# Performance work log

Measured on AMD Instinct MI355X. Metric: run time of the kernel, lower is better.

Reference implementation:

```python
import jax, jax.numpy as jnp
import numpy as np

B, S, T, E, H, VIN, VOUT = 64, 64, 32, 512, 1024, 32000, 32000


def setup_inputs() -> dict:
    key = jax.random.key(0)
    ks = jax.random.split(key, 12)
    rn = lambda k, shape, s=0.02: jax.random.normal(k, shape, jnp.float32) * s
    return {
        "src": jax.random.randint(ks[0], (B, S), 0, VIN),
        "tgt": jax.random.randint(ks[1], (B, T), 0, VOUT),
        "enc_emb": rn(ks[2], (VIN, E)),
        "dec_emb": rn(ks[3], (VOUT, E)),
        "enc_Wih": rn(ks[4], (4 * H, E)),
        "enc_Whh": rn(ks[5], (4 * H, H)),
        "enc_bih": jnp.zeros((4 * H,), jnp.float32),
        "enc_bhh": jnp.zeros((4 * H,), jnp.float32),
        "dec_Wih": rn(ks[6], (4 * H, E + H)),
        "dec_Whh": rn(ks[7], (4 * H, H)),
        "dec_bih": jnp.zeros((4 * H,), jnp.float32),
        "dec_bhh": jnp.zeros((4 * H,), jnp.float32),
        "attn_W": rn(ks[8], (H, 2 * H)),
        "attn_b": jnp.zeros((H,), jnp.float32),
        "v": jax.random.uniform(ks[9], (H,), jnp.float32),
        "fc_W": rn(ks[10], (VOUT, 2 * H)),
        "fc_b": jnp.zeros((VOUT,), jnp.float32),
    }


def _lstm_cell(x, h, c, Wih, Whh, bih, bhh):
    # torch gate order: i, f, g, o
    gates = x @ Wih.T + bih + h @ Whh.T + bhh
    i, f, g, o = jnp.split(gates, 4, axis=-1)
    c_new = jax.nn.sigmoid(f) * c + jax.nn.sigmoid(i) * jnp.tanh(g)
    h_new = jax.nn.sigmoid(o) * jnp.tanh(c_new)
    return h_new, c_new


def _forward(src, tgt, enc_emb, dec_emb, enc_Wih, enc_Whh, enc_bih, enc_bhh,
             dec_Wih, dec_Whh, dec_bih, dec_bhh, attn_W, attn_b, v, fc_W, fc_b):
    b, s = src.shape
    t_len = tgt.shape[1]
    hdim = enc_Whh.shape[1]

    # ---- encoder (single-layer LSTM, batch_first) ----
    x = enc_emb[src]  # [B,S,E] (dropout=0 in eval)

    def enc_step(carry, x_t):
        h, c = carry
        h, c = _lstm_cell(x_t, h, c, enc_Wih, enc_Whh, enc_bih, enc_bhh)
        return (h, c), h

    h0 = jnp.zeros((b, hdim), x.dtype)
    (h_f, c_f), enc_out_tm = jax.lax.scan(enc_step, (h0, h0), jnp.swapaxes(x, 0, 1))
    enc_out = jnp.swapaxes(enc_out_tm, 0, 1)  # [B,S,H]

    # hidden.detach() in torch
    h_f = jax.lax.stop_gradient(h_f)
    c_f = jax.lax.stop_gradient(c_f)

    # split attn_W for the concat(hidden, enc_out) linear
    Wh, We = attn_W[:, :hdim], attn_W[:, hdim:]
    enc_proj = jnp.einsum('bsh,kh->bsk', enc_out, We)  # hoisted, [B,S,H]

    def dec_step(carry, tok):
        h, c = carry
        emb = dec_emb[tok]  # [B,E]
        # Bahdanau attention: tanh(Linear(cat(h, enc_out))) . v
        energy = jnp.tanh(h @ Wh.T[None] if False else jnp.tanh((h @ Wh.T)[:, None, :] + enc_proj + attn_b))
        energy = jnp.tanh((h @ Wh.T)[:, None, :] + enc_proj + attn_b)  # [B,S,H]
        scores = jnp.einsum('bsh,h->bs', energy, v)
        a = jax.nn.softmax(scores, axis=1)
        context = jnp.einsum('bs,bsh->bh', a, enc_out)  # [B,H]
        rnn_in = jnp.concatenate([emb, context], axis=-1)
        h_new, c_new = _lstm_cell(rnn_in, h, c, dec_Wih, dec_Whh, dec_bih, dec_bhh)
        logits = jnp.concatenate([h_new, context], axis=-1) @ fc_W.T + fc_b
        return (h_new, c_new), logits

    # teacher_forcing_ratio = 1.0 -> input at step t is tgt[:, t-1]
    toks_tm = jnp.swapaxes(tgt[:, : t_len - 1], 0, 1)  # [T-1, B]
    _, logits_tm = jax.lax.scan(dec_step, (h_f, c_f), toks_tm)  # [T-1,B,V]
    logits = jnp.swapaxes(logits_tm, 0, 1)  # [B,T-1,V]
    zeros0 = jnp.zeros((b, 1, fc_W.shape[0]), logits.dtype)
    return jnp.concatenate([zeros0, logits], axis=1)  # [B,T,V]


def reference(src, tgt, enc_emb, dec_emb, enc_Wih, enc_Whh, enc_bih, enc_bhh,
              dec_Wih, dec_Whh, dec_bih, dec_bhh, attn_W, attn_b, v, fc_W, fc_b):
    return _forward(src, tgt, enc_emb, dec_emb, enc_Wih, enc_Whh, enc_bih, enc_bhh,
                    dec_Wih, dec_Whh, dec_bih, dec_bhh, attn_W, attn_b, v, fc_W, fc_b)
```

## Files before the change

### kernel.cpp

```cpp
#include <hip/hip_runtime.h>
#include <hip/hip_bf16.h>

typedef __bf16 bf16x8 __attribute__((ext_vector_type(8)));
typedef float  f32x4  __attribute__((ext_vector_type(4)));
typedef _Float16 h16x8 __attribute__((ext_vector_type(8)));

__device__ __forceinline__ unsigned short f2b(float f) {
    union { float f; unsigned u; } w; w.f = f;
    unsigned u = w.u + 0x7FFF + ((w.u >> 16) & 1);
    return (unsigned short)(u >> 16);
}
__device__ __forceinline__ float tanhfast(float x) {
    float e = __expf(2.0f * x);
    return 1.0f - 2.0f / (e + 1.0f);
}

__device__ __forceinline__ void stU(unsigned* p, unsigned v) {
    __hip_atomic_store(p, v, __ATOMIC_RELAXED, __HIP_MEMORY_SCOPE_AGENT);
}
__device__ __forceinline__ void stF(float* p, float v) {
    __hip_atomic_store(p, v, __ATOMIC_RELAXED, __HIP_MEMORY_SCOPE_AGENT);
}
__device__ __forceinline__ int ldI(const int* p) {
    return __hip_atomic_load((int*)p, __ATOMIC_RELAXED, __HIP_MEMORY_SCOPE_AGENT);
}
__device__ __forceinline__ void stI(int* p, int v) {
    __hip_atomic_store(p, v, __ATOMIC_RELAXED, __HIP_MEMORY_SCOPE_AGENT);
}

#define GLD16(g, l) __builtin_amdgcn_global_load_lds( \
    (const __attribute__((address_space(1))) void*)(g), \
    (__attribute__((address_space(3))) void*)(l), 16, 0, 0)

#define SLOT_STRIDE 16

__device__ __forceinline__ void gbar(int* slots, int* gen, int target) {
    asm volatile("s_waitcnt vmcnt(0)" ::: "memory");
    __syncthreads();
    if (blockIdx.x == 0) {
        if (threadIdx.x == 0) stI(slots, target);
        while (ldI(slots + threadIdx.x * SLOT_STRIDE) < target)
            __builtin_amdgcn_s_sleep(1);
        __syncthreads();
        if (threadIdx.x == 0) stI(gen, target);
    } else {
        if (threadIdx.x == 0) {
            stI(slots + blockIdx.x * SLOT_STRIDE, target);
            while (ldI(gen) < target)
                __builtin_amdgcn_s_sleep(1);
        }
        __syncthreads();
    }
}

__device__ __forceinline__ void mac8(const unsigned short* A, const unsigned short* B,
                                     f32x4& acc) {
    bf16x8 a[8], b[8];
#pragma unroll
    for (int kk = 0; kk < 8; ++kk) {
        a[kk] = *(const bf16x8*)(A + kk * 32);
        b[kk] = *(const bf16x8*)(B + kk * 32);
    }
#pragma unroll
    for (int kk = 0; kk < 8; ++kk)
        acc = __builtin_amdgcn_mfma_f32_16x16x32_bf16(a[kk], b[kk], acc, 0, 0, 0);
}


__global__ void k_gather(const float* __restrict__ emb, const int* __restrict__ tok,
                         unsigned short* __restrict__ out, int L, int ldtok) {
    long total = (long)L * 64 * 128;
    for (long i = (long)blockIdx.x * blockDim.x + threadIdx.x; i < total;
         i += (long)gridDim.x * blockDim.x) {
        int  e4 = (int)(i & 127);
        long r  = i >> 7;
        int  t  = (int)(r >> 6), b = (int)(r & 63);
        int  tk = tok[b * ldtok + t];
        float4 v = *(const float4*)(emb + (long)tk * 512 + e4 * 4);
        ushort4 o; o.x = f2b(v.x); o.y = f2b(v.y); o.z = f2b(v.z); o.w = f2b(v.w);
        *(ushort4*)(out + r * 512 + e4 * 4) = o;
    }
}

__global__ void k_conv(const float* __restrict__ in, unsigned short* __restrict__ out,
                       long N_, int K_, int ldin, int col0, int ldout, int outcol0, int reorder) {
    long total = N_ * (K_ >> 2);
    int kq = K_ >> 2;
    for (long i = (long)blockIdx.x * blockDim.x + threadIdx.x; i < total;
         i += (long)gridDim.x * blockDim.x) {
        long n = i / kq;
        int  k4 = (int)(i - n * kq) * 4;
        long row = reorder ? (long)((n & 3) * 1024 + (n >> 2)) : n;
        float4 v = *(const float4*)(in + row * ldin + col0 + k4);
        ushort4 o; o.x = f2b(v.x); o.y = f2b(v.y); o.z = f2b(v.z); o.w = f2b(v.w);
        *(ushort4*)(out + n * ldout + outcol0 + k4) = o;
    }
}

__global__ void k_bias(const float* __restrict__ b1, const float* __restrict__ b2,
                       float* __restrict__ out) {
    int n = blockIdx.x * blockDim.x + threadIdx.x;
    if (n < 4096) {
        int row = (n & 3) * 1024 + (n >> 2);
        out[n] = b1[row] + b2[row];
    }
}

__global__ void k_zero0(float* __restrict__ out) {
    long total = 64L * 8000;
    for (long i = (long)blockIdx.x * blockDim.x + threadIdx.x; i < total;
         i += (long)gridDim.x * blockDim.x) {
        int b = (int)(i / 8000), q = (int)(i % 8000);
        float4 z = {0.f, 0.f, 0.f, 0.f};
        *(float4*)(out + (long)b * 1024000 + q * 4) = z;
    }
}

template<int BM, int BN, int WGM, int WGN, int FM, int FN>
__device__ __forceinline__ void gemm_core(
    const unsigned short* __restrict__ A, int lda,
    const unsigned short* __restrict__ B, int ldb,
    long m0, long n0, int K,
    unsigned short* As, unsigned short* Bs,
    f32x4 (&acc)[FM][FN])
{
    const int tid  = threadIdx.x;
    const int lane = tid & 63;
    const int wave = tid >> 6;
    const int wm = wave / WGN;
    const int wn = wave % WGN;
    const int srow = lane >> 2;
    const int scol = (lane & 3) * 8;
    const int frow = lane & 15;
    const int fcol = (lane >> 4) * 8;

    for (int k0 = 0; k0 < K; k0 += 32) {
        __syncthreads();
        for (int c = wave; c < BM / 16; c += 4) {
            const unsigned short* g = A + (m0 + c * 16 + srow) * (long)lda + k0 + scol;
            GLD16(g, As + c * 512);
        }
        for (int c = wave; c < BN / 16; c += 4) {
            const unsigned short* g = B + (n0 + c * 16 + srow) * (long)ldb + k0 + scol;
            GLD16(g, Bs + c * 512);
        }
        __syncthreads();
        bf16x8 af[FM], bfr[FN];
#pragma unroll
        for (int m = 0; m < FM; ++m)
            af[m] = *(const bf16x8*)(As + ((wm * FM + m) * 16 + frow) * 32 + fcol);
#pragma unroll
        for (int n = 0; n < FN; ++n)
            bfr[n] = *(const bf16x8*)(Bs + ((wn * FN + n) * 16 + frow) * 32 + fcol);
#pragma unroll
        for (int m = 0; m < FM; ++m)
#pragma unroll
            for (int n = 0; n < FN; ++n)
                acc[m][n] = __builtin_amdgcn_mfma_f32_16x16x32_bf16(af[m], bfr[n], acc[m][n], 0, 0, 0);
    }
}

template<int BM, int BN, int WGM, int WGN, int FM, int FN, int MODE>
__global__ __launch_bounds__(256) void k_gemm(
    const unsigned short* __restrict__ A, int lda,
    const unsigned short* __restrict__ B, int ldb,
    float* __restrict__ C, long ldc, const float* __restrict__ bias,
    int M, int N, int K, int Mreal)
{
    __shared__ __align__(16) unsigned short As[BM * 32];
    __shared__ __align__(16) unsigned short Bs[BN * 32];
    long m0, n0;
    if (MODE == 1) {
        int bid = blockIdx.x;
        int n = (bid & 7) * 32 + (bid >> 7);
        int m = (bid >> 3) & 15;
        if (n >= 250) return;
        m0 = (long)m * BM; n0 = (long)n * BN;
    } else {
        m0 = (long)blockIdx.y * BM; n0 = (long)blockIdx.x * BN;
    }
    f32x4 acc[FM][FN] = {};
    gemm_core<BM, BN, WGM, WGN, FM, FN>(A, lda, B, ldb, m0, n0, K, As, Bs, acc);

    const int lane = threadIdx.x & 63;
    const int wave = threadIdx.x >> 6;
    const int wm = wave / WGN, wn = wave % WGN;
#pragma unroll
    for (int n = 0; n < FN; ++n) {
        long col = n0 + wn * FN * 16 + n * 16 + (lane & 15);
        float bv = bias ? bias[col] : 0.0f;
#pragma unroll
        for (int m = 0; m < FM; ++m) {
            int rl = wm * FM * 16 + m * 16 + (lane >> 4) * 4;
#pragma unroll
            for (int q = 0; q < 4; ++q) {
                long r = m0 + rl + q;
                float val = acc[m][n][q] + bv;
                if (MODE == 0) {
                    C[r * ldc + col] = val;
                } else if (MODE == 2) {
                    ((_Float16*)C)[r * ldc + col] = (_Float16)val;
                } else {
                    if (r < Mreal) {
                        long orow = (r & 63) * 32 + (r >> 6) + 1;
                        C[orow * ldc + col] = val;
                    }
                }
            }
        }
    }
}

__global__ __launch_bounds__(256) void k_enc(
    const unsigned short* __restrict__ W,
    const float* __restrict__ pre,
    unsigned short* __restrict__ hsl,
    unsigned short* __restrict__ enc_out,
    unsigned short* __restrict__ eoT,
    unsigned short* __restrict__ hS0,
    float* __restrict__ cspill,
    int* slots, int* gen)
{
    __shared__ float gs[64 * 16];
    const int blk = blockIdx.x, tid = threadIdx.x;
    const int lane = tid & 63, wave = tid >> 6;
    const int n0 = blk * 16;
    const int arow = wave * 16 + (lane & 15);
    const int kch = (lane >> 4) * 8;
    const unsigned short* Bw = W + (long)(n0 + (lane & 15)) * 1024 + kch;
    const int pb = tid >> 1, pjl = (tid & 1) * 2;
    const int jg = blk * 4 + pjl;
    float c0 = 0.f, c1 = 0.f;
    float4 pr0 = {}, pr1 = {};
    if (tid < 128) {
        pr0 = *(const float4*)(pre + (long)pb * 4096 + n0 + pjl * 4);
        pr1 = *(const float4*)(pre + (long)pb * 4096 + n0 + pjl * 4 + 4);
    }
    int bt = 0;
    for (int t = 0; t < 64; ++t) {
        const unsigned short* Ar = hsl + (long)t * 65536 + (long)arow * 1024 + kch;
        f32x4 acc = {};
        mac8(Ar, Bw, acc);
        mac8(Ar + 256, Bw + 256, acc);
        mac8(Ar + 512, Bw + 512, acc);
        mac8(Ar + 768, Bw + 768, acc);
#pragma unroll
        for (int q = 0; q < 4; ++q)
            gs[(wave * 16 + (lane >> 4) * 4 + q) * 16 + (lane & 15)] = acc[q];
        __syncthreads();
        if (tid < 128) {
            float4 gA = *(const float4*)(gs + pb * 16 + pjl * 4);
            float4 gB = *(const float4*)(gs + pb * 16 + pjl * 4 + 4);
            float h0v, h1v;
            {
                float gi = gA.x + pr0.x, gf = gA.y + pr0.y, gg = gA.z + pr0.z, go = gA.w + pr0.w;
                float i_ = 1.f / (1.f + __expf(-gi)), f_ = 1.f / (1.f + __expf(-gf));
                float g_ = tanhfast(gg), o_ = 1.f / (1.f + __expf(-go));
                c0 = f_ * c0 + i_ * g_; h0v = o_ * tanhfast(c0);
            }
            {
                float gi = gB.x + pr1.x, gf = gB.y + pr1.y, gg = gB.z + pr1.z, go = gB.w + pr1.w;
                float i_ = 1.f / (1.f + __expf(-gi)), f_ = 1.f / (1.f + __expf(-gf));
                float g_ = tanhfast(gg), o_ = 1.f / (1.f + __expf(-go));
                c1 = f_ * c1 + i_ * g_; h1v = o_ * tanhfast(c1);
            }
            unsigned short hb0 = f2b(h0v), hb1 = f2b(h1v);
            unsigned pk = (unsigned)hb0 | ((unsigned)hb1 << 16);
            stU((unsigned*)(hsl + (long)(t + 1) * 65536 + (long)pb * 1024 + jg), pk);
            *(unsigned*)(enc_out + ((long)pb * 64 + t) * 1024 + jg) = pk;
            eoT[((long)pb * 1024 + jg) * 64 + t]     = hb0;
            eoT[((long)pb * 1024 + jg + 1) * 64 + t] = hb1;
            if (t < 63) {
                pr0 = *(const float4*)(pre + (long)(t + 1) * 262144 + (long)pb * 4096 + n0 + pjl * 4);
                pr1 = *(const float4*)(pre + (long)(t + 1) * 262144 + (long)pb * 4096 + n0 + pjl * 4 + 4);
            } else {
                *(unsigned*)(hS0 + (long)pb * 1024 + jg) = pk;
                cspill[(long)pb * 1024 + jg]     = c0;
                cspill[(long)pb * 1024 + jg + 1] = c1;
            }
        }
        gbar(slots, gen, ++bt);
    }
}

__global__ __launch_bounds__(256) void k_dec(
    const unsigned short* __restrict__ Wh,
    const unsigned short* __restrict__ Wc,
    const float* __restrict__ pre,
    const _Float16* __restrict__ proj16,
    const unsigned short* __restrict__ eoT,
    const float* __restrict__ v,
    const float* __restrict__ cspill,
    unsigned short* __restrict__ hS,
    unsigned short* __restrict__ ctxS,
    float* __restrict__ qS,
    unsigned short* __restrict__ fcin,
    int* slots, int* gen)
{
    __shared__ float gs[64 * 16];
    __shared__ float qv[1024], vv[1024];
    __shared__ float sc[64], al[64];
    const int blk = blockIdx.x, tid = threadIdx.x;
    const int lane = tid & 63, wave = tid >> 6;
    const int n0 = blk * 16;
    const int arow = wave * 16 + (lane & 15);
    const int kch = (lane >> 4) * 8;
    const int pb = tid >> 1, pjl = (tid & 1) * 2;
    const int jg = blk * 4 + pjl;
    {
        float4 v4 = *(const float4*)(v + tid * 4);
        *(float4*)(vv + tid * 4) = v4;
    }
    float c0 = 0.f, c1 = 0.f;
    if (tid < 128) {
        c0 = cspill[(long)pb * 1024 + jg];
        c1 = cspill[(long)pb * 1024 + jg + 1];
    }
    __syncthreads();
    int bt = 0;
    for (int t = 0; t < 31; ++t) {
        const unsigned short* hSt   = hS   + (long)t * 65536;
        const unsigned short* ctxSt = ctxS + (long)t * 65536;
        float4 pr0 = {}, pr1 = {};
        if (tid < 128) {
            pr0 = *(const float4*)(pre + (long)t * 262144 + (long)pb * 4096 + n0 + pjl * 4);
            pr1 = *(const float4*)(pre + (long)t * 262144 + (long)pb * 4096 + n0 + pjl * 4 + 4);
        }
        {
            int nq = blk >> 2, mt = blk & 3;
            gs[tid] = 0.f;
            __syncthreads();
            const unsigned short* Ar = hSt + (long)(mt * 16 + (lane & 15)) * 1024 + wave * 256 + kch;
            const unsigned short* Bq = Wh + (long)(nq * 16 + (lane & 15)) * 1024 + wave * 256 + kch;
            f32x4 qa = {};
            mac8(Ar, Bq, qa);
#pragma unroll
            for (int q = 0; q < 4; ++q)
                atomicAdd(&gs[((lane >> 4) * 4 + q) * 16 + (lane & 15)], qa[q]);
            __syncthreads();
            stF(qS + (long)t * 65536 + (long)(mt * 16 + (tid >> 4)) * 1024 + nq * 16 + (tid & 15),
                gs[tid]);
        }
        gbar(slots, gen, ++bt);
        if (blk < 64) {
            const int b = blk;
            *(float4*)(qv + tid * 4) = *(const float4*)(qS + (long)t * 65536 + (long)b * 1024 + tid * 4);
            __syncthreads();
            int s = tid >> 2, part = tid & 3;
            const h16x8* pp = (const h16x8*)(proj16 + ((long)b * 64 + s) * 1024 + part * 256);
            float a_ = 0.f;
#pragma unroll 4
            for (int d = 0; d < 32; ++d) {
                h16x8 pv = pp[d];
                int h = part * 256 + d * 8;
#pragma unroll
                for (int j = 0; j < 8; ++j)
                    a_ += vv[h + j] * tanhfast(qv[h + j] + (float)pv[j]);
            }
            a_ += __shfl_xor(a_, 1);
            a_ += __shfl_xor(a_, 2);
            if (part == 0) sc[s] = a_;
            __syncthreads();
            if (tid < 64) {
                float x = sc[tid], mx = x;
                for (int o = 32; o; o >>= 1) mx = fmaxf(mx, __shfl_xor(mx, o));
                float e = __expf(x - mx), su = e;
                for (int o = 32; o; o >>= 1) su += __shfl_xor(su, o);
                al[tid] = e / su;
            }
            __syncthreads();
            int h0 = tid * 4;
            float cacc[4];
#pragma unroll
            for (int r = 0; r < 4; ++r) {
                const bf16x8* ep = (const bf16x8*)(eoT + ((long)b * 1024 + h0 + r) * 64);
                float s_ = 0.f;
#pragma unroll
                for (int c8 = 0; c8 < 8; ++c8) {
                    bf16x8 v8 = ep[c8];
#pragma unroll
                    for (int jj = 0; jj < 8; ++jj)
                        s_ += al[c8 * 8 + jj] * (float)v8[jj];
                }
                cacc[r] = s_;
            }
            unsigned pk0 = (unsigned)f2b(cacc[0]) | ((unsigned)f2b(cacc[1]) << 16);
            unsigned pk1 = (unsigned)f2b(cacc[2]) | ((unsigned)f2b(cacc[3]) << 16);
            stU((unsigned*)(ctxS + (long)t * 65536 + (long)b * 1024 + h0), pk0);
            stU((unsigned*)(ctxS + (long)t * 65536 + (long)b * 1024 + h0 + 2), pk1);
            *(unsigned*)(fcin + ((long)t * 64 + b) * 2048 + 1024 + h0)     = pk0;
            *(unsigned*)(fcin + ((long)t * 64 + b) * 2048 + 1024 + h0 + 2) = pk1;
        }
        gbar(slots, gen, ++bt);
        {
            const unsigned short* Ah = hSt   + (long)arow * 1024 + kch;
            const unsigned short* Ac = ctxSt + (long)arow * 1024 + kch;
            const unsigned short* Bw = Wc + (long)(n0 + (lane & 15)) * 2048 + kch;
            f32x4 acc = {};
            mac8(Ah,       Bw,        acc);
            mac8(Ah + 256, Bw + 256,  acc);
            mac8(Ah + 512, Bw + 512,  acc);
            mac8(Ah + 768, Bw + 768,  acc);
            mac8(Ac,       Bw + 1024, acc);
            mac8(Ac + 256, Bw + 1280, acc);
            mac8(Ac + 512, Bw + 1536, acc);
            mac8(Ac + 768, Bw + 1792, acc);
#pragma unroll
            for (int q = 0; q < 4; ++q)
                gs[(wave * 16 + (lane >> 4) * 4 + q) * 16 + (lane & 15)] = acc[q];
            __syncthreads();
            if (tid < 128) {
                float4 gA = *(const float4*)(gs + pb * 16 + pjl * 4);
                float4 gB = *(const float4*)(gs + pb * 16 + pjl * 4 + 4);
                float h0v, h1v;
                {
                    float gi = gA.x + pr0.x, gf = gA.y + pr0.y, gg = gA.z + pr0.z, go = gA.w + pr0.w;
                    float i_ = 1.f / (1.f + __expf(-gi)), f_ = 1.f / (1.f + __expf(-gf));
                    float g_ = tanhfast(gg), o_ = 1.f / (1.f + __expf(-go));
                    c0 = f_ * c0 + i_ * g_; h0v = o_ * tanhfast(c0);
                }
                {
                    float gi = gB.x + pr1.x, gf = gB.y + pr1.y, gg = gB.z + pr1.z, go = gB.w + pr1.w;
                    float i_ = 1.f / (1.f + __expf(-gi)), f_ = 1.f / (1.f + __expf(-gf));
                    float g_ = tanhfast(gg), o_ = 1.f / (1.f + __expf(-go));
                    c1 = f_ * c1 + i_ * g_; h1v = o_ * tanhfast(c1);
                }
                unsigned pk = (unsigned)f2b(h0v) | ((unsigned)f2b(h1v) << 16);
                stU((unsigned*)(hS + (long)(t + 1) * 65536 + (long)pb * 1024 + jg), pk);
                *(unsigned*)(fcin + ((long)t * 64 + pb) * 2048 + jg) = pk;
            }
        }
        gbar(slots, gen, ++bt);
    }
}

extern "C" void kernel_launch(void* const* d_in, const int* in_sizes, int n_in,
                              void* d_out, int out_size, void* d_ws, size_t ws_size,
                              hipStream_t stream) {
    const int*   src     = (const int*)d_in[0];
    const int*   tgt     = (const int*)d_in[1];
    const float* enc_emb = (const float*)d_in[2];
    const float* dec_emb = (const float*)d_in[3];
    const float* enc_Wih = (const float*)d_in[4];
    const float* enc_Whh = (const float*)d_in[5];
    const float* enc_bih = (const float*)d_in[6];
    const float* enc_bhh = (const float*)d_in[7];
    const float* dec_Wih = (const float*)d_in[8];
    const float* dec_Whh = (const float*)d_in[9];
    const float* dec_bih = (const float*)d_in[10];
    const float* dec_bhh = (const float*)d_in[11];
    const float* attn_W  = (const float*)d_in[12];
    const float* attn_b  = (const float*)d_in[13];
    const float* vvec    = (const float*)d_in[14];
    const float* fc_W    = (const float*)d_in[15];
    const float* fc_b    = (const float*)d_in[16];
    float* out = (float*)d_out;

    char* ws = (char*)d_ws;
    size_t off = 0;
    auto alloc = [&](size_t bytes) -> char* {
        off = (off + 255) & ~(size_t)255;
        char* p = ws + off; off += bytes; return p;
    };
    unsigned short* wX      = (unsigned short*)alloc(4096UL * 512 * 2);
    unsigned short* weWih   = (unsigned short*)alloc(4096UL * 512 * 2);
    unsigned short* weWhh   = (unsigned short*)alloc(4096UL * 1024 * 2);
    float*          ebias   = (float*)alloc(4096UL * 4);
    float*          pre_enc = (float*)alloc(4096UL * 4096 * 4);
    unsigned short* enc_out = (unsigned short*)alloc(4096UL * 1024 * 2);
    unsigned short* eoT     = (unsigned short*)alloc(64UL * 1024 * 64 * 2);
    unsigned short* wWe     = (unsigned short*)alloc(1024UL * 1024 * 2);
    unsigned short* wWh     = (unsigned short*)alloc(1024UL * 1024 * 2);
    _Float16*       proj16  = (_Float16*)alloc(4096UL * 1024 * 2);
    float*          cbuf    = (float*)alloc(64UL * 1024 * 4);
    unsigned short* demb    = (unsigned short*)alloc(2048UL * 512 * 2);
    unsigned short* wDemb   = (unsigned short*)alloc(4096UL * 512 * 2);
    unsigned short* wCat    = (unsigned short*)alloc(4096UL * 2048 * 2);
    float*          dbias   = (float*)alloc(4096UL * 4);
    float*          pre_dec = (float*)alloc(2048UL * 4096 * 4);
    unsigned short* fcin    = (unsigned short*)alloc(2048UL * 2048 * 2);
    unsigned short* wFc     = (unsigned short*)alloc(32000UL * 2048 * 2);
    unsigned short* hslE    = (unsigned short*)alloc(65UL * 65536 * 2);
    unsigned short* hS      = (unsigned short*)alloc(32UL * 65536 * 2);
    unsigned short* ctxS    = (unsigned short*)alloc(32UL * 65536 * 2);
    float*          qS      = (float*)alloc(32UL * 65536 * 4);
    int*            bar     = (int*)alloc(65536);
    (void)ws_size; (void)in_sizes; (void)n_in; (void)out_size;

    int* slotsE = bar;
    int* genE   = bar + 4096;
    int* slotsD = bar + 8192;
    int* genD   = bar + 12288;

    hipMemsetAsync(bar, 0, 65536, stream);
    hipMemsetAsync(hslE, 0, 65536UL * 2, stream);
    k_zero0<<<512, 256, 0, stream>>>(out);

    k_gather<<<2048, 256, 0, stream>>>(enc_emb, src, wX, 64, 64);
    k_gather<<<1024, 256, 0, stream>>>(dec_emb, tgt, demb, 31, 32);
    k_conv<<<2048, 256, 0, stream>>>(enc_Wih, weWih, 4096, 512, 512, 0, 512, 0, 1);
    k_conv<<<2048, 256, 0, stream>>>(enc_Whh, weWhh, 4096, 1024, 1024, 0, 1024, 0, 1);
    k_conv<<<2048, 256, 0, stream>>>(dec_Wih, wDemb, 4096, 512, 1536, 0, 512, 0, 1);
    k_conv<<<2048, 256, 0, stream>>>(dec_Whh, wCat, 4096, 1024, 1024, 0, 2048, 0, 1);
    k_conv<<<2048, 256, 0, stream>>>(dec_Wih, wCat, 4096, 1024, 1536, 512, 2048, 1024, 1);
    k_conv<<<2048, 256, 0, stream>>>(attn_W, wWh, 1024, 1024, 2048, 0, 1024, 0, 0);
    k_conv<<<2048, 256, 0, stream>>>(attn_W, wWe, 1024, 1024, 2048, 1024, 1024, 0, 0);
    k_conv<<<4096, 256, 0, stream>>>(fc_W, wFc, 32000, 2048, 2048, 0, 2048, 0, 0);
    k_bias<<<16, 256, 0, stream>>>(enc_bih, enc_bhh, ebias);
    k_bias<<<16, 256, 0, stream>>>(dec_bih, dec_bhh, dbias);

    k_gemm<128,128,2,2,4,4,0><<<dim3(32, 32), 256, 0, stream>>>(
        wX, 512, weWih, 512, pre_enc, 4096, ebias, 4096, 4096, 512, 4096);
    k_gemm<128,128,2,2,4,4,0><<<dim3(32, 16), 256, 0, stream>>>(
        demb, 512, wDemb, 512, pre_dec, 4096, dbias, 2048, 4096, 512, 2048);

    k_enc<<<256, 256, 0, stream>>>(weWhh, pre_enc, hslE, enc_out, eoT,
                                   hS, cbuf, slotsE, genE);

    k_gemm<128,128,2,2,4,4,2><<<dim3(8, 32), 256, 0, stream>>>(
        enc_out, 1024, wWe, 1024, (float*)proj16, 1024, attn_b, 4096, 1024, 1024, 4096);

    k_dec<<<256, 256, 0, stream>>>(wWh, wCat, pre_dec, proj16, eoT, vvec, cbuf,
                                   hS, ctxS, qS, fcin, slotsD, genD);

    k_gemm<128,128,2,2,4,4,1><<<dim3(4096), 256, 0, stream>>>(
        fcin, 2048, wFc, 2048, out, 32000, fc_b, 2048, 32000, 2048, 1984);
}
```

Measured before the change: 2.680 ms.

## Double threads per block in persistent LSTM kernels via split-K across wave pairs

The persistent encoder and decoder kernels now launch 512 threads per block instead of 256. Each pair of waves splits the K dimension of the recurrent matvec, and the halves are combined in shared memory with a store followed by an atomic add. The attention score and context loops are re-partitioned across the extra threads. The aim is to shorten per-step latency on the serial critical path, at the cost of an extra shared-memory sync and LDS atomics each step, plus higher register pressure under launch_bounds(512,2).

```diff
diff --git a/kernel.cpp b/kernel.cpp
--- a/kernel.cpp
+++ b/kernel.cpp
@@ -33,14 +33,17 @@
     (__attribute__((address_space(3))) void*)(l), 16, 0, 0)
 
 #define SLOT_STRIDE 16
+#define NPOLL 256
 
 __device__ __forceinline__ void gbar(int* slots, int* gen, int target) {
     asm volatile("s_waitcnt vmcnt(0)" ::: "memory");
     __syncthreads();
     if (blockIdx.x == 0) {
         if (threadIdx.x == 0) stI(slots, target);
-        while (ldI(slots + threadIdx.x * SLOT_STRIDE) < target)
-            __builtin_amdgcn_s_sleep(1);
+        if (threadIdx.x < NPOLL) {
+            while (ldI(slots + threadIdx.x * SLOT_STRIDE) < target)
+                __builtin_amdgcn_s_sleep(1);
+        }
         __syncthreads();
         if (threadIdx.x == 0) stI(gen, target);
     } else {
@@ -63,6 +66,18 @@
     }
 #pragma unroll
     for (int kk = 0; kk < 8; ++kk)
+        acc = __builtin_amdgcn_mfma_f32_16x16x32_bf16(a[kk], b[kk], acc, 0, 0, 0);
+}
+__device__ __forceinline__ void mac4(const unsigned short* A, const unsigned short* B,
+                                     f32x4& acc) {
+    bf16x8 a[4], b[4];
+#pragma unroll
+    for (int kk = 0; kk < 4; ++kk) {
+        a[kk] = *(const bf16x8*)(A + kk * 32);
+        b[kk] = *(const bf16x8*)(B + kk * 32);
+    }
+#pragma unroll
+    for (int kk = 0; kk < 4; ++kk)
         acc = __builtin_amdgcn_mfma_f32_16x16x32_bf16(a[kk], b[kk], acc, 0, 0, 0);
 }
 
@@ -211,7 +226,7 @@
     }
 }
 
-__global__ __launch_bounds__(256) void k_enc(
+__global__ __launch_bounds__(512, 2) void k_enc(
     const unsigned short* __restrict__ W,
     const float* __restrict__ pre,
     unsigned short* __restrict__ hsl,
@@ -224,9 +239,11 @@
     __shared__ float gs[64 * 16];
     const int blk = blockIdx.x, tid = threadIdx.x;
     const int lane = tid & 63, wave = tid >> 6;
+    const int rt = wave >> 1, kh = wave & 1;
     const int n0 = blk * 16;
-    const int arow = wave * 16 + (lane & 15);
-    const int kch = (lane >> 4) * 8;
+    const int arow = rt * 16 + (lane & 15);
+    const int kch = kh * 512 + (lane >> 4) * 8;
+    const int grow = (rt * 16 + (lane >> 4) * 4) * 16 + (lane & 15);
     const unsigned short* Bw = W + (long)(n0 + (lane & 15)) * 1024 + kch;
     const int pb = tid >> 1, pjl = (tid & 1) * 2;
     const int jg = blk * 4 + pjl;
@@ -242,11 +259,15 @@
         f32x4 acc = {};
         mac8(Ar, Bw, acc);
         mac8(Ar + 256, Bw + 256, acc);
-        mac8(Ar + 512, Bw + 512, acc);
-        mac8(Ar + 768, Bw + 768, acc);
-#pragma unroll
-        for (int q = 0; q < 4; ++q)
-            gs[(wave * 16 + (lane >> 4) * 4 + q) * 16 + (lane & 15)] = acc[q];
+        if (kh == 0) {
+#pragma unroll
+            for (int q = 0; q < 4; ++q) gs[grow + q * 16] = acc[q];
+        }
+        __syncthreads();
+        if (kh == 1) {
+#pragma unroll
+            for (int q = 0; q < 4; ++q) atomicAdd(&gs[grow + q * 16], acc[q]);
+        }
         __syncthreads();
         if (tid < 128) {
             float4 gA = *(const float4*)(gs + pb * 16 + pjl * 4);
@@ -283,7 +304,7 @@
     }
 }
 
-__global__ __launch_bounds__(256) void k_dec(
+__global__ __launch_bounds__(512, 2) void k_dec(
     const unsigned short* __restrict__ Wh,
     const unsigned short* __restrict__ Wc,
     const float* __restrict__ pre,
@@ -302,12 +323,12 @@
     __shared__ float sc[64], al[64];
     const int blk = blockIdx.x, tid = threadIdx.x;
     const int lane = tid & 63, wave = tid >> 6;
+    const int rt = wave >> 1, kh = wave & 1;
     const int n0 = blk * 16;
-    const int arow = wave * 16 + (lane & 15);
-    const int kch = (lane >> 4) * 8;
+    const int grow = (rt * 16 + (lane >> 4) * 4) * 16 + (lane & 15);
     const int pb = tid >> 1, pjl = (tid & 1) * 2;
     const int jg = blk * 4 + pjl;
-    {
+    if (tid < 256) {
         float4 v4 = *(const float4*)(v + tid * 4);
         *(float4*)(vv + tid * 4) = v4;
     }
@@ -328,37 +349,43 @@
         }
         {
             int nq = blk >> 2, mt = blk & 3;
-            gs[tid] = 0.f;
-            __syncthreads();
-            const unsigned short* Ar = hSt + (long)(mt * 16 + (lane & 15)) * 1024 + wave * 256 + kch;
-            const unsigned short* Bq = Wh + (long)(nq * 16 + (lane & 15)) * 1024 + wave * 256 + kch;
+            if (tid < 256) gs[tid] = 0.f;
+            __syncthreads();
+            const unsigned short* Ar = hSt + (long)(mt * 16 + (lane & 15)) * 1024
+                                           + wave * 128 + (lane >> 4) * 8;
+            const unsigned short* Bq = Wh + (long)(nq * 16 + (lane & 15)) * 1024
+                                          + wave * 128 + (lane >> 4) * 8;
             f32x4 qa = {};
-            mac8(Ar, Bq, qa);
+            mac4(Ar, Bq, qa);
 #pragma unroll
             for (int q = 0; q < 4; ++q)
                 atomicAdd(&gs[((lane >> 4) * 4 + q) * 16 + (lane & 15)], qa[q]);
             __syncthreads();
-            stF(qS + (long)t * 65536 + (long)(mt * 16 + (tid >> 4)) * 1024 + nq * 16 + (tid & 15),
-                gs[tid]);
+            if (tid < 256)
+                stF(qS + (long)t * 65536 + (long)(mt * 16 + (tid >> 4)) * 1024
+                        + nq * 16 + (tid & 15), gs[tid]);
         }
         gbar(slots, gen, ++bt);
         if (blk < 64) {
             const int b = blk;
-            *(float4*)(qv + tid * 4) = *(const float4*)(qS + (long)t * 65536 + (long)b * 1024 + tid * 4);
-            __syncthreads();
-            int s = tid >> 2, part = tid & 3;
-            const h16x8* pp = (const h16x8*)(proj16 + ((long)b * 64 + s) * 1024 + part * 256);
+            if (tid < 256)
+                *(float4*)(qv + tid * 4) =
+                    *(const float4*)(qS + (long)t * 65536 + (long)b * 1024 + tid * 4);
+            __syncthreads();
+            int s = tid >> 3, part = tid & 7;
+            const h16x8* pp = (const h16x8*)(proj16 + ((long)b * 64 + s) * 1024 + part * 128);
             float a_ = 0.f;
 #pragma unroll 4
-            for (int d = 0; d < 32; ++d) {
+            for (int d = 0; d < 16; ++d) {
                 h16x8 pv = pp[d];
-                int h = part * 256 + d * 8;
+                int h = part * 128 + d * 8;
 #pragma unroll
                 for (int j = 0; j < 8; ++j)
                     a_ += vv[h + j] * tanhfast(qv[h + j] + (float)pv[j]);
             }
             a_ += __shfl_xor(a_, 1);
             a_ += __shfl_xor(a_, 2);
+            a_ += __shfl_xor(a_, 4);
             if (part == 0) sc[s] = a_;
             __syncthreads();
             if (tid < 64) {
@@ -369,10 +396,10 @@
                 al[tid] = e / su;
             }
             __syncthreads();
-            int h0 = tid * 4;
-            float cacc[4];
-#pragma unroll
-            for (int r = 0; r < 4; ++r) {
+            int h0 = tid * 2;
+            float cacc[2];
+#pragma unroll
+            for (int r = 0; r < 2; ++r) {
                 const bf16x8* ep = (const bf16x8*)(eoT + ((long)b * 1024 + h0 + r) * 64);
                 float s_ = 0.f;
 #pragma unroll
@@ -385,29 +412,29 @@
                 cacc[r] = s_;
             }
             unsigned pk0 = (unsigned)f2b(cacc[0]) | ((unsigned)f2b(cacc[1]) << 16);
-            unsigned pk1 = (unsigned)f2b(cacc[2]) | ((unsigned)f2b(cacc[3]) << 16);
             stU((unsigned*)(ctxS + (long)t * 65536 + (long)b * 1024 + h0), pk0);
-            stU((unsigned*)(ctxS + (long)t * 65536 + (long)b * 1024 + h0 + 2), pk1);
-            *(unsigned*)(fcin + ((long)t * 64 + b) * 2048 + 1024 + h0)     = pk0;
-            *(unsigned*)(fcin + ((long)t * 64 + b) * 2048 + 1024 + h0 + 2) = pk1;
+            *(unsigned*)(fcin + ((long)t * 64 + b) * 2048 + 1024 + h0) = pk0;
         }
         gbar(slots, gen, ++bt);
         {
-            const unsigned short* Ah = hSt   + (long)arow * 1024 + kch;
-            const unsigned short* Ac = ctxSt + (long)arow * 1024 + kch;
-            const unsigned short* Bw = Wc + (long)(n0 + (lane & 15)) * 2048 + kch;
+            const unsigned short* Asrc = (kh ? ctxSt : hSt)
+                + (long)(rt * 16 + (lane & 15)) * 1024 + (lane >> 4) * 8;
+            const unsigned short* Bw = Wc + (long)(n0 + (lane & 15)) * 2048
+                                          + kh * 1024 + (lane >> 4) * 8;
             f32x4 acc = {};
-            mac8(Ah,       Bw,        acc);
-            mac8(Ah + 256, Bw + 256,  acc);
-            mac8(Ah + 512, Bw + 512,  acc);
-            mac8(Ah + 768, Bw + 768,  acc);
-            mac8(Ac,       Bw + 1024, acc);
-            mac8(Ac + 256, Bw + 1280, acc);
-            mac8(Ac + 512, Bw + 1536, acc);
-            mac8(Ac + 768, Bw + 1792, acc);
-#pragma unroll
-            for (int q = 0; q < 4; ++q)
-                gs[(wave * 16 + (lane >> 4) * 4 + q) * 16 + (lane & 15)] = acc[q];
+            mac8(Asrc,       Bw,       acc);
+            mac8(Asrc + 256, Bw + 256, acc);
+            mac8(Asrc + 512, Bw + 512, acc);
+            mac8(Asrc + 768, Bw + 768, acc);
+            if (kh == 0) {
+#pragma unroll
+                for (int q = 0; q < 4; ++q) gs[grow + q * 16] = acc[q];
+            }
+            __syncthreads();
+            if (kh == 1) {
+#pragma unroll
+                for (int q = 0; q < 4; ++q) atomicAdd(&gs[grow + q * 16], acc[q]);
+            }
             __syncthreads();
             if (tid < 128) {
                 float4 gA = *(const float4*)(gs + pb * 16 + pjl * 4);
@@ -514,13 +541,13 @@
     k_gemm<128,128,2,2,4,4,0><<<dim3(32, 16), 256, 0, stream>>>(
         demb, 512, wDemb, 512, pre_dec, 4096, dbias, 2048, 4096, 512, 2048);
 
-    k_enc<<<256, 256, 0, stream>>>(weWhh, pre_enc, hslE, enc_out, eoT,
+    k_enc<<<256, 512, 0, stream>>>(weWhh, pre_enc, hslE, enc_out, eoT,
                                    hS, cbuf, slotsE, genE);
 
     k_gemm<128,128,2,2,4,4,2><<<dim3(8, 32), 256, 0, stream>>>(
         enc_out, 1024, wWe, 1024, (float*)proj16, 1024, attn_b, 4096, 1024, 1024, 4096);
 
-    k_dec<<<256, 256, 0, stream>>>(wWh, wCat, pre_dec, proj16, eoT, vvec, cbuf,
+    k_dec<<<256, 512, 0, stream>>>(wWh, wCat, pre_dec, proj16, eoT, vvec, cbuf,
                                    hS, ctxS, qS, fcin, slotsD, genD);
 
     k_gemm<128,128,2,2,4,4,1><<<dim3(4096), 256, 0, stream>>>(
```

Measured after the change: 2.595 ms. 1.03x faster.
